# Optimization experiments

Hardware: AMD Instinct MI355X
Metric: run time of the kernel (lower is better)

The kernel has to match this reference:

```python
import jax, jax.numpy as jnp
import numpy as np

D_MODEL = 2048
N_HEADS = 16
D_HEAD = 128
N_GROUPS = 4          # KV heads = N_HEADS // N_GROUPS = 4
D_FF = 2048           # hard-coded default in FeedForward
EPS = 1e-6


def setup_inputs() -> dict:
    key = jax.random.key(0)
    ks = jax.random.split(key, 16)
    B, S = 4, 1024
    Hkv = N_HEADS // N_GROUPS
    s = 0.02
    inp = {
        "x": jax.random.normal(ks[0], (B, S, D_MODEL), jnp.float32),
        "scale1": jnp.ones((D_MODEL,), jnp.float32),
        "Wq": jax.random.normal(ks[1], (D_MODEL, N_HEADS * D_HEAD), jnp.float32) * s,
        "bq": jnp.zeros((N_HEADS * D_HEAD,), jnp.float32),
        "Wk": jax.random.normal(ks[2], (D_MODEL, Hkv * D_HEAD), jnp.float32) * s,
        "bk": jnp.zeros((Hkv * D_HEAD,), jnp.float32),
        "Wv": jax.random.normal(ks[3], (D_MODEL, Hkv * D_HEAD), jnp.float32) * s,
        "bv": jnp.zeros((Hkv * D_HEAD,), jnp.float32),
        "Wo": jax.random.normal(ks[4], (N_HEADS * D_HEAD, D_MODEL), jnp.float32) * s,
        "bo": jnp.zeros((D_MODEL,), jnp.float32),
        "W1": jax.random.normal(ks[5], (D_MODEL, D_FF), jnp.float32) * s,
        "b1": jnp.zeros((D_FF,), jnp.float32),
        "W2": jax.random.normal(ks[6], (D_FF, D_MODEL), jnp.float32) * s,
        "b2": jnp.zeros((D_MODEL,), jnp.float32),
    }
    return inp


def _rmsnorm(x, scale):
    rms = jnp.sqrt(jnp.mean(x * x, axis=-1, keepdims=True) + EPS)
    return scale * (x / rms)


def reference(x, scale1, Wq, bq, Wk, bk, Wv, bv, Wo, bo, W1, b1, W2, b2):
    B, S, _ = x.shape
    Hkv = N_HEADS // N_GROUPS
    xn = _rmsnorm(x, scale1)  # [B,S,D]

    # GQA attention (prefill, step=None -> no cache)
    Q = (xn @ Wq + bq).reshape(B, S, N_HEADS, D_HEAD).transpose(0, 2, 1, 3)  # [B,H,S,d]
    K = (xn @ Wk + bk).reshape(B, S, Hkv, D_HEAD).transpose(0, 2, 1, 3)      # [B,Hkv,S,d]
    V = (xn @ Wv + bv).reshape(B, S, Hkv, D_HEAD).transpose(0, 2, 1, 3)
    Kr = jnp.repeat(K, N_GROUPS, axis=1)  # [B,H,S,d]
    Vr = jnp.repeat(V, N_GROUPS, axis=1)
    scores = jnp.einsum("bhqd,bhkd->bhqk", Q, Kr) / jnp.sqrt(jnp.float32(D_HEAD))
    attn = jax.nn.softmax(scores, axis=-1)
    out = jnp.einsum("bhqk,bhkd->bhqd", attn, Vr)  # [B,H,S,d]
    out = out.transpose(0, 2, 1, 3).reshape(B, S, N_HEADS * D_HEAD)
    x = x + out @ Wo + bo

    # Source bug preserved: FFN consumes rms_norm1 output, rms_norm2 is dead code
    h = xn @ W1 + b1
    h = h * jax.nn.sigmoid(h) * h  # x_ff * silu(x_ff)
    x = x + h @ W2 + b2
    return x
```

## Files before the change

### kernel.cpp

```cpp
#include <hip/hip_runtime.h>
#include <hip/hip_bf16.h>
#include <cstdint>

using bf16 = __hip_bfloat16;
typedef __attribute__((ext_vector_type(8))) __bf16 bf16x8;
typedef __attribute__((ext_vector_type(4))) float f32x4;

#define MFMA16(a, b, c) __builtin_amdgcn_mfma_f32_16x16x32_bf16((a), (b), (c), 0, 0, 0)

#if __has_builtin(__builtin_amdgcn_exp2f)
__device__ __forceinline__ float fexp2(float x) { return __builtin_amdgcn_exp2f(x); }
#else
__device__ __forceinline__ float fexp2(float x) { return exp2f(x); }
#endif

__device__ __forceinline__ void async16(void* lds_ptr, const void* gptr) {
  auto g = reinterpret_cast<__attribute__((address_space(1))) unsigned int*>(
      reinterpret_cast<uintptr_t>(gptr));
  auto l = reinterpret_cast<__attribute__((address_space(3))) unsigned int*>(
      static_cast<unsigned int>(reinterpret_cast<uintptr_t>(lds_ptr)));
  __builtin_amdgcn_global_load_lds(g, l, 16, 0, 0);
}

__device__ __forceinline__ void tr_body(const float* __restrict__ W,
                                        bf16* __restrict__ Wt, int N, int ldt,
                                        int row_off, int k_off, int lb, int nx,
                                        float (*t)[33], int tx, int ty) {
  const int n0 = (lb % nx) * 32, k0 = (lb / nx) * 32;
#pragma unroll
  for (int i = 0; i < 4; ++i)
    t[ty + 8 * i][tx] = W[(size_t)(k0 + ty + 8 * i) * N + n0 + tx];
  __syncthreads();
#pragma unroll
  for (int i = 0; i < 4; ++i)
    Wt[(size_t)(row_off + n0 + ty + 8 * i) * ldt + k_off + k0 + tx] =
        __float2bfloat16(t[tx][ty + 8 * i]);
}

__global__ __launch_bounds__(256) void prep_k(
    const float* __restrict__ x, const float* __restrict__ s1, bf16* __restrict__ xn,
    const float* __restrict__ Wq, const float* __restrict__ Wk,
    const float* __restrict__ Wv, const float* __restrict__ W1,
    const float* __restrict__ Wo, const float* __restrict__ W2,
    bf16* __restrict__ wcatT, bf16* __restrict__ wcat2T,
    const float* __restrict__ bq, const float* __restrict__ bk,
    const float* __restrict__ bv, const float* __restrict__ b1,
    const float* __restrict__ bo, const float* __restrict__ b2,
    float* __restrict__ bcat) {
  __shared__ float t[32][33];
  const int tid = threadIdx.x;
  int bid = blockIdx.x;
  if (bid < 4096) {
    const int row = bid;
    const float4* xr = (const float4*)(x + (size_t)row * 2048);
    float4 a = xr[tid * 2], b = xr[tid * 2 + 1];
    float ss = a.x * a.x + a.y * a.y + a.z * a.z + a.w * a.w +
               b.x * b.x + b.y * b.y + b.z * b.z + b.w * b.w;
#pragma unroll
    for (int d = 1; d < 64; d <<= 1) ss += __shfl_xor(ss, d);
    if ((tid & 63) == 0) t[0][tid >> 6] = ss;
    __syncthreads();
    const float rinv =
        rsqrtf((t[0][0] + t[0][1] + t[0][2] + t[0][3]) * (1.0f / 2048.0f) + 1e-6f);
    const float4* sp = (const float4*)s1;
    float4 s0 = sp[tid * 2], s1v = sp[tid * 2 + 1];
    union { bf16 h[8]; bf16x8 v; } o;
    o.h[0] = __float2bfloat16(a.x * rinv * s0.x);
    o.h[1] = __float2bfloat16(a.y * rinv * s0.y);
    o.h[2] = __float2bfloat16(a.z * rinv * s0.z);
    o.h[3] = __float2bfloat16(a.w * rinv * s0.w);
    o.h[4] = __float2bfloat16(b.x * rinv * s1v.x);
    o.h[5] = __float2bfloat16(b.y * rinv * s1v.y);
    o.h[6] = __float2bfloat16(b.z * rinv * s1v.z);
    o.h[7] = __float2bfloat16(b.w * rinv * s1v.w);
    *(bf16x8*)(xn + (size_t)row * 2048 + tid * 8) = o.v;
    return;
  }
  if (bid < 4124) {
    const int i = (bid - 4096) * 256 + tid;
    float v;
    if (i < 2048) v = bq[i];
    else if (i < 2560) v = bk[i - 2048];
    else if (i < 3072) v = bv[i - 2560];
    else if (i < 5120) v = b1[i - 3072];
    else v = bo[i - 5120] + b2[i - 5120];
    bcat[i] = v;
    return;
  }
  bid -= 4124;
  const int tx = tid & 31, ty = tid >> 5;
  if (bid < 4096)       tr_body(Wq, wcatT, 2048, 2048, 0, 0, bid, 64, t, tx, ty);
  else if (bid < 5120)  tr_body(Wk, wcatT, 512, 2048, 2048, 0, bid - 4096, 16, t, tx, ty);
  else if (bid < 6144)  tr_body(Wv, wcatT, 512, 2048, 2560, 0, bid - 5120, 16, t, tx, ty);
  else if (bid < 10240) tr_body(W1, wcatT, 2048, 2048, 3072, 0, bid - 6144, 64, t, tx, ty);
  else if (bid < 14336) tr_body(Wo, wcat2T, 2048, 4096, 0, 0, bid - 10240, 64, t, tx, ty);
  else                  tr_body(W2, wcat2T, 2048, 4096, 0, 2048, bid - 14336, 64, t, tx, ty);
}

__global__ void transpose_v_k(const bf16* __restrict__ qkv, bf16* __restrict__ vtb) {
  __shared__ bf16 t[32][33];
  const int bh = blockIdx.z, b = bh >> 2, g = bh & 3;
  const int s0 = blockIdx.x * 32, d0 = blockIdx.y * 32;
  const int tx = threadIdx.x, ty = threadIdx.y;
#pragma unroll
  for (int i = 0; i < 4; ++i)
    t[ty + 8 * i][tx] =
        qkv[(size_t)(b * 1024 + s0 + ty + 8 * i) * 3072 + 2560 + g * 128 + d0 + tx];
  __syncthreads();
#pragma unroll
  for (int i = 0; i < 4; ++i)
    vtb[((size_t)bh * 128 + d0 + ty + 8 * i) * 1024 + s0 + tx] = t[tx][ty + 8 * i];
}

#define BARRIER() \
  { asm volatile("" ::: "memory"); __builtin_amdgcn_s_barrier(); asm volatile("" ::: "memory"); }
#define VM_MAIN                                                          \
  { if constexpr (LPS == 4) { asm volatile("s_waitcnt vmcnt(8)" ::: "memory"); } \
    else { asm volatile("s_waitcnt vmcnt(6)" ::: "memory"); } }
#define VM_ONE                                                           \
  { if constexpr (LPS == 4) { asm volatile("s_waitcnt vmcnt(4)" ::: "memory"); } \
    else { asm volatile("s_waitcnt vmcnt(3)" ::: "memory"); } }
#define VM_ZERO \
  { asm volatile("s_waitcnt vmcnt(0)" ::: "memory"); }

#define READ_AF(MILO)                                                              \
  { unsigned char* ab_ = lds + (h_ & 3) * SLOTA;                                   \
    _Pragma("unroll") for (int i_ = 0; i_ < MI / 2; ++i_) {                        \
      const int R_ = arow0 + ((MILO) + i_) * 16;                                   \
      af[i_] = *(const bf16x8*)(ab_ + R_ * 64 + ((hi ^ ((R_ >> 1) & 3)) << 4)); } }

#define READ_BF()                                                                  \
  { unsigned char* bb_ = lds + 4 * SLOTA + (h_ & 3) * SLOTB;                       \
    _Pragma("unroll") for (int j_ = 0; j_ < NJ; ++j_) {                            \
      const int S_ = bcol0 + j_ * 16;                                              \
      bf[j_] = *(const bf16x8*)(bb_ + S_ * 64 + ((hi ^ ((S_ >> 1) & 3)) << 4)); } }

#define MFMA_HALF(MILO)                                                            \
  __builtin_amdgcn_s_setprio(1);                                                   \
  _Pragma("unroll") for (int i_ = 0; i_ < MI / 2; ++i_)                            \
    _Pragma("unroll") for (int j_ = 0; j_ < NJ; ++j_)                              \
      acc[(MILO) + i_][j_] = MFMA16(af[i_], bf[j_], acc[(MILO) + i_][j_]);         \
  __builtin_amdgcn_s_setprio(0);

#define GSLOT(H, DOSTG, VMSTMT)                                                    \
  { const int h_ = (H);                                                            \
    if (DOSTG) { stgA(h_ + 3); stgB(h_ + 3); }                                     \
    READ_AF(0); READ_BF();                                                         \
    MFMA_HALF(0);                                                                  \
    READ_AF(MI / 2);                                                               \
    MFMA_HALF(MI / 2);                                                             \
    VMSTMT;                                                                        \
    BARRIER(); }

template <int MI, int NJ, int WM, int WN, int EPI>
__global__ __launch_bounds__(512, 2) void gemm8(
    const bf16* __restrict__ A, const bf16* __restrict__ A2,
    const bf16* __restrict__ Bt, const float* __restrict__ bias,
    const float* __restrict__ res, void* __restrict__ out0,
    void* __restrict__ out1, int K) {
  constexpr int BM = WM * MI * 16;
  constexpr int BN = WN * NJ * 16;
  constexpr int SLOTA = BM * 64;
  constexpr int SLOTB = BN * 64;
  constexpr int NSWA = SLOTA / 8192;
  constexpr int NSWB = SLOTB / 8192;
  constexpr int FRACB = SLOTB % 8192;
  constexpr int LPS = NSWA + NSWB;
  extern __shared__ unsigned char lds[];

  const int tid = threadIdx.x, lane = tid & 63, w = tid >> 6;
  const int wr = w / WN, wc = w % WN;
  const int hi = lane >> 4, lo = lane & 15;

  const int lid = blockIdx.y * 16 + blockIdx.x;
  const int xj = lid & 7, jj = lid >> 3;
  const int brow = ((xj & 3) * 4 + (jj & 3)) * BM;
  const int bcol = ((xj >> 2) * 8 + (jj >> 2)) * BN;

  const int NS = K >> 5;

  size_t offA[NSWA];
#pragma unroll
  for (int i = 0; i < NSWA; ++i) {
    const int o = i * 8192 + tid * 16;
    const int r = o >> 6;
    const int c = ((((o >> 4) & 3) ^ ((r >> 1) & 3)) << 3);
    offA[i] = (size_t)(brow + r) * 2048 + c;
  }
  const bf16* srcB[NSWB + (FRACB ? 1 : 0)];
#pragma unroll
  for (int i = 0; i < NSWB + (FRACB ? 1 : 0); ++i) {
    const int o = i * 8192 + tid * 16;
    const int r = o >> 6;
    const int c = ((((o >> 4) & 3) ^ ((r >> 1) & 3)) << 3);
    srcB[i] = Bt + (size_t)(bcol + r) * K + c;
  }

  auto stgA = [&](int h) {
    unsigned char* ab = lds + (h & 3) * SLOTA;
    const int kb = h * 32;
    const bf16* base;
    int ko;
    if constexpr (EPI == 1) { base = (kb < 2048) ? A : A2; ko = kb & 2047; }
    else { base = A; ko = kb; }
#pragma unroll
    for (int i = 0; i < NSWA; ++i)
      async16(ab + i * 8192 + tid * 16, base + offA[i] + ko);
  };
  auto stgB = [&](int h) {
    unsigned char* bb = lds + 4 * SLOTA + (h & 3) * SLOTB;
    const int kb = h * 32;
#pragma unroll
    for (int i = 0; i < NSWB; ++i)
      async16(bb + i * 8192 + tid * 16, srcB[i] + kb);
    if constexpr (FRACB != 0) {
      if (tid < FRACB / 16)
        async16(bb + NSWB * 8192 + tid * 16, srcB[NSWB] + kb);
    }
  };

  const int arow0 = wr * (MI * 16) + lo;
  const int bcol0 = wc * (NJ * 16) + lo;

  stgA(0); stgB(0); stgA(1); stgB(1); stgA(2); stgB(2);
  VM_MAIN;
  BARRIER();

  f32x4 acc[MI][NJ] = {};
  bf16x8 af[MI / 2], bf[NJ];

  for (int h = 0; h < NS - 3; ++h) { GSLOT(h, true, VM_MAIN); }
  GSLOT(NS - 3, false, VM_ONE);
  GSLOT(NS - 2, false, VM_ZERO);
  GSLOT(NS - 1, false, (void)0);

#pragma unroll
  for (int mi = 0; mi < MI; ++mi) {
    const int row = brow + wr * (MI * 16) + mi * 16 + hi * 4;
#pragma unroll
    for (int nj = 0; nj < NJ; ++nj) {
      const int col = bcol + wc * (NJ * 16) + nj * 16 + lo;
      const float bs = bias[col];
#pragma unroll
      for (int r = 0; r < 4; ++r) {
        float v = acc[mi][nj][r] + bs;
        if constexpr (EPI == 0) {
          if (col < 3072) {
            ((bf16*)out0)[(size_t)(row + r) * 3072 + col] = __float2bfloat16(v);
          } else {
            const float sg = 1.0f / (1.0f + __expf(-v));
            ((bf16*)out1)[(size_t)(row + r) * 2048 + (col - 3072)] =
                __float2bfloat16(v * sg * v);
          }
        } else {
          v += res[(size_t)(row + r) * 2048 + col];
          ((float*)out0)[(size_t)(row + r) * 2048 + col] = v;
        }
      }
    }
  }
}

__global__ __launch_bounds__(256, 4) void attn_fwd(
    const bf16* __restrict__ qkv, const bf16* __restrict__ vtb, bf16* __restrict__ out) {
  __shared__ __align__(16) unsigned char alds[40960];
  unsigned char* Ks = alds;
  unsigned char* Vs = alds + 16384;
  unsigned char* Ps = alds + 32768;
  const int tid = threadIdx.x, lane = tid & 63, w = tid >> 6;
  const int hi = lane >> 4, lo = lane & 15;
  const int qt = blockIdx.x, bh = blockIdx.y;
  const int b = bh >> 4, h = bh & 15, g = h >> 2;
  const size_t tok0 = (size_t)b * 1024;
  const int q0 = qt * 64;

  bf16x8 qf[4];
  {
    const bf16* qp = qkv + (tok0 + q0 + w * 16 + lo) * 3072 + h * 128 + hi * 8;
#pragma unroll
    for (int kc = 0; kc < 4; ++kc) qf[kc] = *(const bf16x8*)(qp + kc * 32);
  }

  float m2 = -1e30f, lsum = 0.f;
  f32x4 oacc[8] = {};
  const float c2 = 0.08838834764831845f * 1.44269504088896f;

  const int o = tid * 16;
  const bf16* kbase = qkv + tok0 * 3072 + 2048 + g * 128;
  const bf16* vbase = vtb + (size_t)(b * 4 + g) * 128 * 1024;
  unsigned char* Pw = Ps + w * 2048;

  for (int t = 0; t < 16; ++t) {
    const int kb = t * 64;
#pragma unroll
    for (int rd = 0; rd < 4; ++rd) {
      const int oo = o + rd * 4096;
      const int rK = oo >> 8, cK = ((oo >> 4) & 15) ^ (rK & 15);
      const int rV = oo >> 7, cV = ((oo >> 4) & 7) ^ (rV & 7);
      async16(Ks + oo, kbase + (size_t)(kb + rK) * 3072 + cK * 8);
      async16(Vs + oo, vbase + (size_t)rV * 1024 + kb + cV * 8);
    }
    __syncthreads();

    f32x4 sc[4] = {};
    __builtin_amdgcn_s_setprio(1);
#pragma unroll
    for (int kc = 0; kc < 4; ++kc) {
#pragma unroll
      for (int kg = 0; kg < 4; ++kg) {
        const int row = kg * 16 + lo;
        bf16x8 kf = *(const bf16x8*)(Ks + row * 256 + ((((kc << 2) + hi) ^ (row & 15)) << 4));
        sc[kg] = MFMA16(kf, qf[kc], sc[kg]);
      }
    }
    __builtin_amdgcn_s_setprio(0);

    float mx = sc[0][0];
#pragma unroll
    for (int kg = 0; kg < 4; ++kg)
#pragma unroll
      for (int r = 0; r < 4; ++r) mx = fmaxf(mx, sc[kg][r]);
    mx = fmaxf(mx, __shfl_xor(mx, 16));
    mx = fmaxf(mx, __shfl_xor(mx, 32));
    mx *= c2;
    const float mn = fmaxf(m2, mx);
    const float corr = fexp2(m2 - mn);
    m2 = mn;

    float rs = 0.f;
#pragma unroll
    for (int kg = 0; kg < 4; ++kg) {
      union { bf16 hh[4]; uint2 v; } pk;
#pragma unroll
      for (int r = 0; r < 4; ++r) {
        const float p = fexp2(sc[kg][r] * c2 - mn);
        rs += p;
        pk.hh[r] = __float2bfloat16(p);
      }
      *(uint2*)(Pw + lo * 128 + ((((kg << 1) + (hi >> 1)) ^ (lo & 7)) << 4) +
                ((hi & 1) << 3)) = pk.v;
    }
    rs += __shfl_xor(rs, 16);
    rs += __shfl_xor(rs, 32);
    lsum = lsum * corr + rs;

    float corr_r[4];
#pragma unroll
    for (int r = 0; r < 4; ++r) corr_r[r] = __shfl(corr, hi * 4 + r);
#pragma unroll
    for (int dg = 0; dg < 8; ++dg)
#pragma unroll
      for (int r = 0; r < 4; ++r) oacc[dg][r] *= corr_r[r];

    asm volatile("s_waitcnt lgkmcnt(0)" ::: "memory");

    bf16x8 pf[2];
#pragma unroll
    for (int kc = 0; kc < 2; ++kc)
      pf[kc] = *(const bf16x8*)(Pw + lo * 128 + ((((kc << 2) + hi) ^ (lo & 7)) << 4));
    __builtin_amdgcn_s_setprio(1);
#pragma unroll
    for (int dg = 0; dg < 8; ++dg) {
#pragma unroll
      for (int kc = 0; kc < 2; ++kc) {
        const int vrow = dg * 16 + lo;
        bf16x8 vf = *(const bf16x8*)(Vs + vrow * 128 + ((((kc << 2) + hi) ^ (vrow & 7)) << 4));
        oacc[dg] = MFMA16(pf[kc], vf, oacc[dg]);
      }
    }
    __builtin_amdgcn_s_setprio(0);
    __syncthreads();
  }

  const float linv = 1.0f / lsum;
  float lr[4];
#pragma unroll
  for (int r = 0; r < 4; ++r) lr[r] = __shfl(linv, hi * 4 + r);
  bf16* op = out + (tok0 + q0 + w * 16 + hi * 4) * 2048 + h * 128 + lo;
#pragma unroll
  for (int dg = 0; dg < 8; ++dg)
#pragma unroll
    for (int r = 0; r < 4; ++r)
      op[(size_t)r * 2048 + dg * 16] = __float2bfloat16(oacc[dg][r] * lr[r]);
}

extern "C" void kernel_launch(void* const* d_in, const int* in_sizes, int n_in,
                              void* d_out, int out_size, void* d_ws, size_t ws_size,
                              hipStream_t stream) {
  (void)in_sizes; (void)n_in; (void)out_size; (void)ws_size;
  const float* x  = (const float*)d_in[0];
  const float* s1 = (const float*)d_in[1];
  const float* Wq = (const float*)d_in[2];
  const float* bq = (const float*)d_in[3];
  const float* Wk = (const float*)d_in[4];
  const float* bk = (const float*)d_in[5];
  const float* Wv = (const float*)d_in[6];
  const float* bv = (const float*)d_in[7];
  const float* Wo = (const float*)d_in[8];
  const float* bo = (const float*)d_in[9];
  const float* W1 = (const float*)d_in[10];
  const float* b1 = (const float*)d_in[11];
  const float* W2 = (const float*)d_in[12];
  const float* b2 = (const float*)d_in[13];
  float* outp = (float*)d_out;

  char* ws = (char*)d_ws;
  bf16*  xn     = (bf16*)(ws + 0);
  bf16*  vtb    = (bf16*)(ws + 0);
  bf16*  wcatT  = (bf16*)(ws + 16777216);
  bf16*  attnb  = (bf16*)(ws + 16777216);
  float* bcat   = (float*)(ws + 37748736);
  bf16*  wcat2T = (bf16*)(ws + 37781504);
  bf16*  qkvb   = (bf16*)(ws + 54558720);
  bf16*  gbuf   = (bf16*)(ws + 79724544);

  prep_k<<<dim3(22556), dim3(256), 0, stream>>>(
      x, s1, xn, Wq, Wk, Wv, W1, Wo, W2, wcatT, wcat2T,
      bq, bk, bv, b1, bo, b2, bcat);
  gemm8<8, 5, 2, 4, 0><<<dim3(16, 16), dim3(512), 147456, stream>>>(
      xn, xn, wcatT, bcat, (const float*)nullptr, (void*)qkvb, (void*)gbuf, 2048);
  transpose_v_k<<<dim3(32, 4, 16), dim3(32, 8), 0, stream>>>(qkvb, vtb);
  attn_fwd<<<dim3(16, 64), dim3(256), 0, stream>>>(qkvb, vtb, attnb);
  gemm8<4, 4, 4, 2, 1><<<dim3(16, 16), dim3(512), 98304, stream>>>(
      attnb, gbuf, wcat2T, bcat + 5120, x, (void*)outp, (void*)nullptr, 4096);
}
```

Measured before the change: 245.1 us.

## Replace 4-stage 512-thread GEMM with double-buffered 256-thread smaller-tile GEMM

Replaces the 8-wave, 4-slot LDS pipelined GEMM with a 4-wave kernel that uses two LDS buffers and fixed 128-wide N tiles. Block tile sizes shrink, so each GEMM launches more blocks (640 and 512 instead of 256), and the blocks-to-XCD mapping becomes generic over the grid shape. The intent is better occupancy and CU fill with less LDS per block. In exchange, prefetch depth drops to one stage and every iteration waits for all outstanding loads (vmcnt(0)), which can expose global-memory latency and lower reuse per block.

Result: slower. 496.1 us (+102.4%).

```diff
diff --git a/kernel.cpp b/kernel.cpp
--- a/kernel.cpp
+++ b/kernel.cpp
@@ -21,6 +21,9 @@
       static_cast<unsigned int>(reinterpret_cast<uintptr_t>(lds_ptr)));
   __builtin_amdgcn_global_load_lds(g, l, 16, 0, 0);
 }
+
+#define BARRIER() \
+  { asm volatile("" ::: "memory"); __builtin_amdgcn_s_barrier(); asm volatile("" ::: "memory"); }
 
 __device__ __forceinline__ void tr_body(const float* __restrict__ W,
                                         bf16* __restrict__ Wt, int N, int ldt,
@@ -112,92 +115,51 @@
     vtb[((size_t)bh * 128 + d0 + ty + 8 * i) * 1024 + s0 + tx] = t[tx][ty + 8 * i];
 }
 
-#define BARRIER() \
-  { asm volatile("" ::: "memory"); __builtin_amdgcn_s_barrier(); asm volatile("" ::: "memory"); }
-#define VM_MAIN                                                          \
-  { if constexpr (LPS == 4) { asm volatile("s_waitcnt vmcnt(8)" ::: "memory"); } \
-    else { asm volatile("s_waitcnt vmcnt(6)" ::: "memory"); } }
-#define VM_ONE                                                           \
-  { if constexpr (LPS == 4) { asm volatile("s_waitcnt vmcnt(4)" ::: "memory"); } \
-    else { asm volatile("s_waitcnt vmcnt(3)" ::: "memory"); } }
-#define VM_ZERO \
-  { asm volatile("s_waitcnt vmcnt(0)" ::: "memory"); }
-
-#define READ_AF(MILO)                                                              \
-  { unsigned char* ab_ = lds + (h_ & 3) * SLOTA;                                   \
-    _Pragma("unroll") for (int i_ = 0; i_ < MI / 2; ++i_) {                        \
-      const int R_ = arow0 + ((MILO) + i_) * 16;                                   \
-      af[i_] = *(const bf16x8*)(ab_ + R_ * 64 + ((hi ^ ((R_ >> 1) & 3)) << 4)); } }
-
-#define READ_BF()                                                                  \
-  { unsigned char* bb_ = lds + 4 * SLOTA + (h_ & 3) * SLOTB;                       \
-    _Pragma("unroll") for (int j_ = 0; j_ < NJ; ++j_) {                            \
-      const int S_ = bcol0 + j_ * 16;                                              \
-      bf[j_] = *(const bf16x8*)(bb_ + S_ * 64 + ((hi ^ ((S_ >> 1) & 3)) << 4)); } }
-
-#define MFMA_HALF(MILO)                                                            \
-  __builtin_amdgcn_s_setprio(1);                                                   \
-  _Pragma("unroll") for (int i_ = 0; i_ < MI / 2; ++i_)                            \
-    _Pragma("unroll") for (int j_ = 0; j_ < NJ; ++j_)                              \
-      acc[(MILO) + i_][j_] = MFMA16(af[i_], bf[j_], acc[(MILO) + i_][j_]);         \
-  __builtin_amdgcn_s_setprio(0);
-
-#define GSLOT(H, DOSTG, VMSTMT)                                                    \
-  { const int h_ = (H);                                                            \
-    if (DOSTG) { stgA(h_ + 3); stgB(h_ + 3); }                                     \
-    READ_AF(0); READ_BF();                                                         \
-    MFMA_HALF(0);                                                                  \
-    READ_AF(MI / 2);                                                               \
-    MFMA_HALF(MI / 2);                                                             \
-    VMSTMT;                                                                        \
-    BARRIER(); }
-
-template <int MI, int NJ, int WM, int WN, int EPI>
-__global__ __launch_bounds__(512, 2) void gemm8(
+template <int MI, int EPI>
+__global__ __launch_bounds__(256, 3) void gemm_db(
     const bf16* __restrict__ A, const bf16* __restrict__ A2,
     const bf16* __restrict__ Bt, const float* __restrict__ bias,
     const float* __restrict__ res, void* __restrict__ out0,
     void* __restrict__ out1, int K) {
-  constexpr int BM = WM * MI * 16;
-  constexpr int BN = WN * NJ * 16;
+  constexpr int BM = 2 * MI * 16;
+  constexpr int BN = 128;
   constexpr int SLOTA = BM * 64;
   constexpr int SLOTB = BN * 64;
-  constexpr int NSWA = SLOTA / 8192;
-  constexpr int NSWB = SLOTB / 8192;
-  constexpr int FRACB = SLOTB % 8192;
-  constexpr int LPS = NSWA + NSWB;
+  constexpr int NSWA = SLOTA / 4096;
+  constexpr int NSWB = 2;
   extern __shared__ unsigned char lds[];
 
   const int tid = threadIdx.x, lane = tid & 63, w = tid >> 6;
-  const int wr = w / WN, wc = w % WN;
+  const int wr = w >> 1, wc = w & 1;
   const int hi = lane >> 4, lo = lane & 15;
 
-  const int lid = blockIdx.y * 16 + blockIdx.x;
-  const int xj = lid & 7, jj = lid >> 3;
-  const int brow = ((xj & 3) * 4 + (jj & 3)) * BM;
-  const int bcol = ((xj >> 2) * 8 + (jj >> 2)) * BN;
+  const int lid = blockIdx.y * gridDim.x + blockIdx.x;
+  const int rpx = gridDim.x >> 3;
+  const int xcd = lid & 7, jj = lid >> 3;
+  const int brow = (xcd * rpx + (jj % rpx)) * BM;
+  const int bcol = (jj / rpx) * BN;
 
   const int NS = K >> 5;
 
   size_t offA[NSWA];
 #pragma unroll
   for (int i = 0; i < NSWA; ++i) {
-    const int o = i * 8192 + tid * 16;
+    const int o = i * 4096 + tid * 16;
     const int r = o >> 6;
     const int c = ((((o >> 4) & 3) ^ ((r >> 1) & 3)) << 3);
     offA[i] = (size_t)(brow + r) * 2048 + c;
   }
-  const bf16* srcB[NSWB + (FRACB ? 1 : 0)];
-#pragma unroll
-  for (int i = 0; i < NSWB + (FRACB ? 1 : 0); ++i) {
-    const int o = i * 8192 + tid * 16;
+  const bf16* srcB[NSWB];
+#pragma unroll
+  for (int i = 0; i < NSWB; ++i) {
+    const int o = i * 4096 + tid * 16;
     const int r = o >> 6;
     const int c = ((((o >> 4) & 3) ^ ((r >> 1) & 3)) << 3);
     srcB[i] = Bt + (size_t)(bcol + r) * K + c;
   }
 
   auto stgA = [&](int h) {
-    unsigned char* ab = lds + (h & 3) * SLOTA;
+    unsigned char* ab = lds + (h & 1) * SLOTA;
     const int kb = h * 32;
     const bf16* base;
     int ko;
@@ -205,41 +167,57 @@
     else { base = A; ko = kb; }
 #pragma unroll
     for (int i = 0; i < NSWA; ++i)
-      async16(ab + i * 8192 + tid * 16, base + offA[i] + ko);
+      async16(ab + i * 4096 + tid * 16, base + offA[i] + ko);
   };
   auto stgB = [&](int h) {
-    unsigned char* bb = lds + 4 * SLOTA + (h & 3) * SLOTB;
+    unsigned char* bb = lds + 2 * SLOTA + (h & 1) * SLOTB;
     const int kb = h * 32;
 #pragma unroll
     for (int i = 0; i < NSWB; ++i)
-      async16(bb + i * 8192 + tid * 16, srcB[i] + kb);
-    if constexpr (FRACB != 0) {
-      if (tid < FRACB / 16)
-        async16(bb + NSWB * 8192 + tid * 16, srcB[NSWB] + kb);
-    }
+      async16(bb + i * 4096 + tid * 16, srcB[i] + kb);
   };
 
   const int arow0 = wr * (MI * 16) + lo;
-  const int bcol0 = wc * (NJ * 16) + lo;
-
-  stgA(0); stgB(0); stgA(1); stgB(1); stgA(2); stgB(2);
-  VM_MAIN;
+  const int bcol0 = wc * 64 + lo;
+
+  stgA(0); stgB(0);
+  asm volatile("s_waitcnt vmcnt(0)" ::: "memory");
   BARRIER();
 
-  f32x4 acc[MI][NJ] = {};
-  bf16x8 af[MI / 2], bf[NJ];
-
-  for (int h = 0; h < NS - 3; ++h) { GSLOT(h, true, VM_MAIN); }
-  GSLOT(NS - 3, false, VM_ONE);
-  GSLOT(NS - 2, false, VM_ZERO);
-  GSLOT(NS - 1, false, (void)0);
+  f32x4 acc[MI][4] = {};
+  bf16x8 af[MI], bf[4];
+
+  for (int h = 0; h < NS; ++h) {
+    if (h + 1 < NS) { stgA(h + 1); stgB(h + 1); }
+    unsigned char* ab = lds + (h & 1) * SLOTA;
+    unsigned char* bb = lds + 2 * SLOTA + (h & 1) * SLOTB;
+#pragma unroll
+    for (int mi = 0; mi < MI; ++mi) {
+      const int R = arow0 + mi * 16;
+      af[mi] = *(const bf16x8*)(ab + R * 64 + ((hi ^ ((R >> 1) & 3)) << 4));
+    }
+#pragma unroll
+    for (int nj = 0; nj < 4; ++nj) {
+      const int S = bcol0 + nj * 16;
+      bf[nj] = *(const bf16x8*)(bb + S * 64 + ((hi ^ ((S >> 1) & 3)) << 4));
+    }
+    __builtin_amdgcn_s_setprio(1);
+#pragma unroll
+    for (int mi = 0; mi < MI; ++mi)
+#pragma unroll
+      for (int nj = 0; nj < 4; ++nj)
+        acc[mi][nj] = MFMA16(af[mi], bf[nj], acc[mi][nj]);
+    __builtin_amdgcn_s_setprio(0);
+    asm volatile("s_waitcnt vmcnt(0)" ::: "memory");
+    BARRIER();
+  }
 
 #pragma unroll
   for (int mi = 0; mi < MI; ++mi) {
     const int row = brow + wr * (MI * 16) + mi * 16 + hi * 4;
 #pragma unroll
-    for (int nj = 0; nj < NJ; ++nj) {
-      const int col = bcol + wc * (NJ * 16) + nj * 16 + lo;
+    for (int nj = 0; nj < 4; ++nj) {
+      const int col = bcol + wc * 64 + nj * 16 + lo;
       const float bs = bias[col];
 #pragma unroll
       for (int r = 0; r < 4; ++r) {
@@ -417,10 +395,10 @@
   prep_k<<<dim3(22556), dim3(256), 0, stream>>>(
       x, s1, xn, Wq, Wk, Wv, W1, Wo, W2, wcatT, wcat2T,
       bq, bk, bv, b1, bo, b2, bcat);
-  gemm8<8, 5, 2, 4, 0><<<dim3(16, 16), dim3(512), 147456, stream>>>(
+  gemm_db<8, 0><<<dim3(16, 40), dim3(256), 49152, stream>>>(
       xn, xn, wcatT, bcat, (const float*)nullptr, (void*)qkvb, (void*)gbuf, 2048);
   transpose_v_k<<<dim3(32, 4, 16), dim3(32, 8), 0, stream>>>(qkvb, vtb);
   attn_fwd<<<dim3(16, 64), dim3(256), 0, stream>>>(qkvb, vtb, attnb);
-  gemm8<4, 4, 4, 2, 1><<<dim3(16, 16), dim3(512), 98304, stream>>>(
+  gemm_db<4, 1><<<dim3(32, 16), dim3(256), 32768, stream>>>(
       attnb, gbuf, wcat2T, bcat + 5120, x, (void*)outp, (void*)nullptr, 4096);
 }
```
